# Kernel tuning notes

Hardware: AMD Instinct MI355X
Metric: run time of the kernel (lower is better)

Reference implementation:

```python
import jax, jax.numpy as jnp
import numpy as np

B, C, K, H, W = 8, 256, 19, 256, 256  # batch, input_nc, num_classes, spatial
NEG_SLOPE = 0.2


def setup_inputs() -> dict:
    key = jax.random.key(0)
    ks = jax.random.split(key, 12)
    x = jax.random.normal(ks[0], (B, C, H, W), jnp.float32)
    cam = jax.random.uniform(ks[1], (B, K, H, W), jnp.float32)
    gt = jax.random.randint(ks[2], (B, K), 0, 3, jnp.int32)
    gt_src = jax.random.uniform(ks[3], (B, K, K), jnp.float32)
    gt_tgt = jax.random.uniform(ks[4], (B, K, K), jnp.float32)
    weights = jax.random.uniform(ks[5], (B, K), jnp.float32)
    W1 = jax.random.normal(ks[6], (C, 2048), jnp.float32) * 0.02
    b1 = jnp.zeros((2048,), jnp.float32)
    W2 = jax.random.normal(ks[7], (2048, 512), jnp.float32) * 0.02
    b2 = jnp.zeros((512,), jnp.float32)
    Wc = jax.random.normal(ks[8], (512, 2 * K), jnp.float32) * 0.02
    bc = jnp.zeros((2 * K,), jnp.float32)
    return {"x": x, "cam": cam, "gt": gt, "gt_src": gt_src, "gt_tgt": gt_tgt,
            "weights": weights, "W1": W1, "b1": b1, "W2": W2, "b2": b2,
            "Wc": Wc, "bc": bc}


def reference(x, cam, gt, gt_src, gt_tgt, weights, W1, b1, W2, b2, Wc, bc):
    hw = x.shape[-1] * x.shape[-2]
    # cams_feature: mean over HW of cam[:,:,None]*x[:,None] -> [B, K, C]
    feat = jnp.einsum('bkhw,bchw->bkc', cam, x) / hw
    # Small MLP (self.D) + cls head, batched over all B*K rows; masking
    # replaces the per-sample ragged gather (extra rows are masked out below).
    h = jax.nn.leaky_relu(feat @ W1 + b1, NEG_SLOPE)
    h = jax.nn.leaky_relu(h @ W2 + b2, NEG_SLOPE)
    logits = h @ Wc + bc                      # [B, K, 2K]
    mask = (gt > 0).astype(logits.dtype)      # [B, K] selected rows
    lbl = jnp.concatenate([gt_src, gt_tgt], axis=-1)  # [B, K, 2K]
    logp = jax.nn.log_softmax(logits, axis=-1)
    ce = -(lbl * logp).sum(-1)                # [B, K]
    n = mask.sum(-1)                          # rows per sample
    sample_loss = (mask * weights * ce).sum(-1) / jnp.maximum(n, 1.0)
    lbl_sum = (mask[..., None] * lbl).sum((-2, -1))   # per-sample label mass
    valid = lbl_sum > 0                       # skip samples with lbl.sum()==0
    batch_size = x.shape[0]
    loss_img = jnp.where(valid, sample_loss, 0.0).sum() / batch_size
    match = (jnp.argmax(logits, -1) == jnp.argmax(lbl, -1)).astype(logits.dtype) * mask
    acc = jnp.where(valid, match.sum(-1), 0.0).sum()
    cnt = jnp.where(valid, lbl_sum, 0.0).sum()
    acc_img = acc / cnt * 100.0
    return jnp.stack([loss_img, acc_img])
```

## Files before the change

### kernel.cpp

```cpp
#include <hip/hip_runtime.h>
#include <stdint.h>

#define BB 8
#define CC 256
#define KK 19
#define HWN 65536
#define H1 2048
#define H2 512
#define NC 38
#define NEG 0.2f
#define NSL 16
#define HWS (HWN / NSL)
#define HWT 256
#define NCH (HWS / HWT)
#define CAMF4 (KK * HWT / 4)
#define NROW (BB * KK)

typedef float nat4 __attribute__((ext_vector_type(4)));

__device__ __forceinline__ void gload_lds16(const float4* g, float4* l) {
    __builtin_amdgcn_global_load_lds(
        (const __attribute__((address_space(1))) void*)g,
        (__attribute__((address_space(3))) void*)l, 16, 0, 0);
}

__global__ __launch_bounds__(256) void k_feat(const float* __restrict__ x,
                                              const float* __restrict__ cam,
                                              const int* __restrict__ gt,
                                              float* __restrict__ partial) {
    __shared__ float cams[2][KK * HWT];
    const int b  = blockIdx.y;
    const int cg = blockIdx.x & 15;
    const int sl = blockIdx.x >> 4;
    const int t  = threadIdx.x;
    const int w  = t >> 6;
    const int l  = t & 63;
    const int c0 = cg * 16 + w * 4;

    unsigned gtm = 0;
#pragma unroll
    for (int k = 0; k < KK; ++k)
        gtm |= (gt[b * KK + k] > 0) ? (1u << k) : 0u;

    const nat4*  __restrict__ x4  = reinterpret_cast<const nat4*>(x);
    const float4* __restrict__ cb4 = reinterpret_cast<const float4*>(cam) + (size_t)b * KK * (HWN / 4);
    const int slbase = sl * (HWS / 4);

    float acc[KK][4];
#pragma unroll
    for (int k = 0; k < KK; ++k)
#pragma unroll
        for (int c = 0; c < 4; ++c) acc[k][c] = 0.f;

    auto stage = [&](int buf, int ch) {
        const int f0 = slbase + ch * (HWT / 4);
#pragma unroll
        for (int j = 0; j < 5; ++j) {
            const int idx = w * 64 + j * 256;
            const int row = idx >> 6;
            if (idx < CAMF4 && ((gtm >> row) & 1)) {
                gload_lds16(cb4 + (size_t)row * (HWN / 4) + f0 + l,
                            ((float4*)cams[buf]) + idx + l);
            }
        }
    };
    auto loadx = [&](nat4 (&xv)[4], int ch) {
        const int f0 = slbase + ch * (HWT / 4);
#pragma unroll
        for (int c = 0; c < 4; ++c)
            xv[c] = __builtin_nontemporal_load(
                x4 + (size_t)(b * CC + c0 + c) * (HWN / 4) + f0 + l);
    };
    auto consume = [&](int buf, const nat4 (&xv)[4]) {
        const float4* cs = (const float4*)cams[buf];
#pragma unroll
        for (int k = 0; k < KK; ++k) {
            if ((gtm >> k) & 1) {
                const float4 cv = cs[k * (HWT / 4) + l];
#pragma unroll
                for (int c = 0; c < 4; ++c)
                    acc[k][c] = fmaf(xv[c].w, cv.w, fmaf(xv[c].z, cv.z,
                                fmaf(xv[c].y, cv.y, fmaf(xv[c].x, cv.x, acc[k][c]))));
            }
        }
    };

    nat4 xa[4], xb[4];
    loadx(xa, 0);
    stage(0, 0);
    __syncthreads();

#pragma unroll 1
    for (int ch = 0; ch < NCH; ch += 2) {
        loadx(xb, ch + 1);
        stage(1, ch + 1);
        consume(0, xa);
        __syncthreads();
        if (ch + 2 < NCH) { loadx(xa, ch + 2); stage(0, ch + 2); }
        consume(1, xb);
        __syncthreads();
    }

#pragma unroll
    for (int k = 0; k < KK; ++k) {
#pragma unroll
        for (int c = 0; c < 4; ++c) {
            float v = acc[k][c];
#pragma unroll
            for (int off = 32; off; off >>= 1) v += __shfl_xor(v, off, 64);
            if (l == 0)
                __builtin_nontemporal_store(v,
                    partial + (size_t)sl * (NROW * CC) +
                    (size_t)(b * KK + k) * CC + c0 + c);
        }
    }
}

__global__ __launch_bounds__(256) void k_mlp1(const float* __restrict__ partial,
                                              const float* __restrict__ W1,
                                              const float* __restrict__ b1,
                                              float* __restrict__ h1,
                                              float* __restrict__ scal) {
    __shared__ float fr[2][CC];
    const int r0 = blockIdx.y * 2;
    const int t  = threadIdx.x;
    if (blockIdx.x == 0 && blockIdx.y == 0 && t < 16) scal[t] = 0.f;

    float s0 = 0.f, s1 = 0.f;
#pragma unroll
    for (int slc = 0; slc < NSL; ++slc) {
        s0 += partial[((size_t)slc * NROW + r0) * CC + t];
        s1 += partial[((size_t)slc * NROW + r0 + 1) * CC + t];
    }
    fr[0][t] = s0 * (1.0f / (float)HWN);
    fr[1][t] = s1 * (1.0f / (float)HWN);
    __syncthreads();

    const int j = blockIdx.x * 256 + t;
    const float4* f0 = (const float4*)fr[0];
    const float4* f1 = (const float4*)fr[1];
    const float bias = b1[j];
    float a0 = bias, a1 = bias;
#pragma unroll 8
    for (int c4 = 0; c4 < CC / 4; ++c4) {
        const float4 v0 = f0[c4], v1 = f1[c4];
        const size_t cb = (size_t)(c4 * 4) * H1 + j;
        const float w0 = W1[cb], w1 = W1[cb + H1], w2 = W1[cb + 2 * H1], w3 = W1[cb + 3 * H1];
        a0 = fmaf(v0.x, w0, a0); a0 = fmaf(v0.y, w1, a0); a0 = fmaf(v0.z, w2, a0); a0 = fmaf(v0.w, w3, a0);
        a1 = fmaf(v1.x, w0, a1); a1 = fmaf(v1.y, w1, a1); a1 = fmaf(v1.z, w2, a1); a1 = fmaf(v1.w, w3, a1);
    }
    h1[(size_t)r0 * H1 + j]       = a0 > 0.f ? a0 : NEG * a0;
    h1[(size_t)(r0 + 1) * H1 + j] = a1 > 0.f ? a1 : NEG * a1;
}

__global__ __launch_bounds__(128) void k_mlp2p(const float* __restrict__ h1,
                                               const float* __restrict__ W2,
                                               float* __restrict__ part) {
    const int j  = blockIdx.x * 128 + threadIdx.x;
    const int r0 = blockIdx.y * 2;
    const int cb = blockIdx.z * 512;
    const float4* __restrict__ f0 = reinterpret_cast<const float4*>(h1 + (size_t)r0 * H1 + cb);
    const float4* __restrict__ f1 = reinterpret_cast<const float4*>(h1 + (size_t)(r0 + 1) * H1 + cb);

    float a0 = 0.f, a1 = 0.f;
#pragma unroll 8
    for (int c4 = 0; c4 < 128; ++c4) {
        const float4 v0 = f0[c4], v1 = f1[c4];
        const size_t wb = (size_t)(cb + c4 * 4) * H2 + j;
        const float w0 = W2[wb], w1 = W2[wb + H2], w2 = W2[wb + 2 * H2], w3 = W2[wb + 3 * H2];
        a0 = fmaf(v0.x, w0, a0); a0 = fmaf(v0.y, w1, a0); a0 = fmaf(v0.z, w2, a0); a0 = fmaf(v0.w, w3, a0);
        a1 = fmaf(v1.x, w0, a1); a1 = fmaf(v1.y, w1, a1); a1 = fmaf(v1.z, w2, a1); a1 = fmaf(v1.w, w3, a1);
    }
    part[((size_t)blockIdx.z * NROW + r0) * H2 + j]     = a0;
    part[((size_t)blockIdx.z * NROW + r0 + 1) * H2 + j] = a1;
}

__global__ __launch_bounds__(768) void k_loss(const float* __restrict__ part,
                                              const float* __restrict__ b2,
                                              const float* __restrict__ Wc,
                                              const float* __restrict__ bc,
                                              const int* __restrict__ gt,
                                              const float* __restrict__ gt_src,
                                              const float* __restrict__ gt_tgt,
                                              const float* __restrict__ wts,
                                              float* __restrict__ scal) {
    __shared__ float h2s[KK][H2];
    __shared__ float lg[KK][NC];
    __shared__ float rloss[KK], rmask[KK], rlbl[KK], rmatch[KK];

    const int b = blockIdx.x;
    const int t = threadIdx.x;

    for (int i = t; i < KK * H2; i += 768) {
        const int row = b * KK + (i >> 9);
        const int jj  = i & 511;
        float s = b2[jj];
#pragma unroll
        for (int p = 0; p < 4; ++p)
            s += part[((size_t)p * NROW + row) * H2 + jj];
        ((float*)h2s)[i] = s > 0.f ? s : NEG * s;
    }
    __syncthreads();

    if (t < KK * NC) {
        const int k = t / NC, j = t % NC;
        float acc = bc[j];
        for (int c = 0; c < H2; ++c) acc = fmaf(h2s[k][c], Wc[(size_t)c * NC + j], acc);
        lg[k][j] = acc;
    }
    __syncthreads();

    if (t < KK) {
        const int k = t;
        float m = -1e30f; int am = 0;
        for (int j = 0; j < NC; ++j) {
            float v = lg[k][j];
            if (v > m) { m = v; am = j; }
        }
        float se = 0.f, celbl = 0.f, lsum = 0.f, lm = -1e30f; int al = 0;
        for (int j = 0; j < NC; ++j) {
            float v = lg[k][j];
            se += expf(v - m);
            float lb = (j < KK) ? gt_src[((size_t)b * KK + k) * KK + j]
                                : gt_tgt[((size_t)b * KK + k) * KK + (j - KK)];
            celbl = fmaf(lb, v, celbl);
            lsum += lb;
            if (lb > lm) { lm = lb; al = j; }
        }
        float lse = m + logf(se);
        float ce = lse * lsum - celbl;
        float mask = (gt[b * KK + k] > 0) ? 1.f : 0.f;
        rloss[k]  = mask * wts[b * KK + k] * ce;
        rmask[k]  = mask;
        rlbl[k]   = mask * lsum;
        rmatch[k] = mask * ((am == al) ? 1.f : 0.f);
    }
    __syncthreads();

    if (t == 0) {
        float n = 0.f, sl = 0.f, ls = 0.f, mt = 0.f;
        for (int k = 0; k < KK; ++k) { n += rmask[k]; sl += rloss[k]; ls += rlbl[k]; mt += rmatch[k]; }
        float sample_loss = sl / fmaxf(n, 1.f);
        bool valid = ls > 0.f;
        atomicAdd(&scal[0], valid ? sample_loss : 0.f);
        atomicAdd(&scal[1], valid ? mt : 0.f);
        atomicAdd(&scal[2], valid ? ls : 0.f);
    }
}

__global__ void k_final(const float* __restrict__ scal, float* __restrict__ out) {
    out[0] = scal[0] / (float)BB;
    out[1] = scal[1] / scal[2] * 100.f;
}

extern "C" void kernel_launch(void* const* d_in, const int* in_sizes, int n_in,
                              void* d_out, int out_size, void* d_ws, size_t ws_size,
                              hipStream_t stream) {
    const float* x      = (const float*)d_in[0];
    const float* cam    = (const float*)d_in[1];
    const int*   gt     = (const int*)d_in[2];
    const float* gt_src = (const float*)d_in[3];
    const float* gt_tgt = (const float*)d_in[4];
    const float* wts    = (const float*)d_in[5];
    const float* W1     = (const float*)d_in[6];
    const float* b1     = (const float*)d_in[7];
    const float* W2     = (const float*)d_in[8];
    const float* b2     = (const float*)d_in[9];
    const float* Wc     = (const float*)d_in[10];
    const float* bc     = (const float*)d_in[11];

    float* ws      = (float*)d_ws;
    float* scal    = ws;
    float* partial = ws + 16;
    float* h1      = partial + (size_t)NSL * NROW * CC;
    float* part2   = h1 + (size_t)NROW * H1;

    dim3 g1(16 * NSL, BB);
    k_feat<<<g1, 256, 0, stream>>>(x, cam, gt, partial);
    dim3 g2(H1 / 256, NROW / 2);
    k_mlp1<<<g2, 256, 0, stream>>>(partial, W1, b1, h1, scal);
    dim3 g3(4, NROW / 2, 4);
    k_mlp2p<<<g3, 128, 0, stream>>>(h1, W2, part2);
    k_loss<<<BB, 768, 0, stream>>>(part2, b2, Wc, bc, gt, gt_src, gt_tgt, wts, scal);
    k_final<<<1, 1, 0, stream>>>(scal, (float*)d_out);
}
```

Measured before the change: 233.9 us.

## Skip masked rows in MLP kernels and halve HW slice count

The two MLP kernels now launch one block per row and return early when gt for that row is not positive, so rows the loss later masks out no longer read weights or do FMAs. The HW split of the feature reduction drops from 16 to 8 slices, which halves the partial-sum traffic but gives the feature kernel fewer blocks and longer per-block loops. Masked rows leave uninitialised h1 and part2 entries, so this is only safe if the loss kernel ignores those rows. Handling one row per block instead of two also means each weight load is reused for only one row.

After: 244.8 us. +4.7%, slower.

```diff
diff --git a/kernel.cpp b/kernel.cpp
--- a/kernel.cpp
+++ b/kernel.cpp
@@ -9,7 +9,7 @@
 #define H2 512
 #define NC 38
 #define NEG 0.2f
-#define NSL 16
+#define NSL 8
 #define HWS (HWN / NSL)
 #define HWT 256
 #define NCH (HWS / HWT)
@@ -119,60 +119,58 @@
 __global__ __launch_bounds__(256) void k_mlp1(const float* __restrict__ partial,
                                               const float* __restrict__ W1,
                                               const float* __restrict__ b1,
+                                              const int* __restrict__ gt,
                                               float* __restrict__ h1,
                                               float* __restrict__ scal) {
-    __shared__ float fr[2][CC];
-    const int r0 = blockIdx.y * 2;
-    const int t  = threadIdx.x;
+    __shared__ float fr[CC];
+    const int r = blockIdx.y;
+    const int t = threadIdx.x;
     if (blockIdx.x == 0 && blockIdx.y == 0 && t < 16) scal[t] = 0.f;
-
-    float s0 = 0.f, s1 = 0.f;
-#pragma unroll
-    for (int slc = 0; slc < NSL; ++slc) {
-        s0 += partial[((size_t)slc * NROW + r0) * CC + t];
-        s1 += partial[((size_t)slc * NROW + r0 + 1) * CC + t];
-    }
-    fr[0][t] = s0 * (1.0f / (float)HWN);
-    fr[1][t] = s1 * (1.0f / (float)HWN);
+    if (gt[r] <= 0) return;
+
+    float s0 = 0.f;
+#pragma unroll
+    for (int slc = 0; slc < NSL; ++slc)
+        s0 += partial[((size_t)slc * NROW + r) * CC + t];
+    fr[t] = s0 * (1.0f / (float)HWN);
     __syncthreads();
 
     const int j = blockIdx.x * 256 + t;
-    const float4* f0 = (const float4*)fr[0];
-    const float4* f1 = (const float4*)fr[1];
-    const float bias = b1[j];
-    float a0 = bias, a1 = bias;
+    const float4* f0 = (const float4*)fr;
+    float a0 = b1[j];
 #pragma unroll 8
     for (int c4 = 0; c4 < CC / 4; ++c4) {
-        const float4 v0 = f0[c4], v1 = f1[c4];
+        const float4 v0 = f0[c4];
         const size_t cb = (size_t)(c4 * 4) * H1 + j;
-        const float w0 = W1[cb], w1 = W1[cb + H1], w2 = W1[cb + 2 * H1], w3 = W1[cb + 3 * H1];
-        a0 = fmaf(v0.x, w0, a0); a0 = fmaf(v0.y, w1, a0); a0 = fmaf(v0.z, w2, a0); a0 = fmaf(v0.w, w3, a0);
-        a1 = fmaf(v1.x, w0, a1); a1 = fmaf(v1.y, w1, a1); a1 = fmaf(v1.z, w2, a1); a1 = fmaf(v1.w, w3, a1);
-    }
-    h1[(size_t)r0 * H1 + j]       = a0 > 0.f ? a0 : NEG * a0;
-    h1[(size_t)(r0 + 1) * H1 + j] = a1 > 0.f ? a1 : NEG * a1;
+        a0 = fmaf(v0.x, W1[cb], a0);
+        a0 = fmaf(v0.y, W1[cb + H1], a0);
+        a0 = fmaf(v0.z, W1[cb + 2 * H1], a0);
+        a0 = fmaf(v0.w, W1[cb + 3 * H1], a0);
+    }
+    h1[(size_t)r * H1 + j] = a0 > 0.f ? a0 : NEG * a0;
 }
 
 __global__ __launch_bounds__(128) void k_mlp2p(const float* __restrict__ h1,
                                                const float* __restrict__ W2,
+                                               const int* __restrict__ gt,
                                                float* __restrict__ part) {
+    const int r = blockIdx.y;
+    if (gt[r] <= 0) return;
     const int j  = blockIdx.x * 128 + threadIdx.x;
-    const int r0 = blockIdx.y * 2;
     const int cb = blockIdx.z * 512;
-    const float4* __restrict__ f0 = reinterpret_cast<const float4*>(h1 + (size_t)r0 * H1 + cb);
-    const float4* __restrict__ f1 = reinterpret_cast<const float4*>(h1 + (size_t)(r0 + 1) * H1 + cb);
-
-    float a0 = 0.f, a1 = 0.f;
+    const float4* __restrict__ f0 = reinterpret_cast<const float4*>(h1 + (size_t)r * H1 + cb);
+
+    float a0 = 0.f;
 #pragma unroll 8
     for (int c4 = 0; c4 < 128; ++c4) {
-        const float4 v0 = f0[c4], v1 = f1[c4];
+        const float4 v0 = f0[c4];
         const size_t wb = (size_t)(cb + c4 * 4) * H2 + j;
-        const float w0 = W2[wb], w1 = W2[wb + H2], w2 = W2[wb + 2 * H2], w3 = W2[wb + 3 * H2];
-        a0 = fmaf(v0.x, w0, a0); a0 = fmaf(v0.y, w1, a0); a0 = fmaf(v0.z, w2, a0); a0 = fmaf(v0.w, w3, a0);
-        a1 = fmaf(v1.x, w0, a1); a1 = fmaf(v1.y, w1, a1); a1 = fmaf(v1.z, w2, a1); a1 = fmaf(v1.w, w3, a1);
-    }
-    part[((size_t)blockIdx.z * NROW + r0) * H2 + j]     = a0;
-    part[((size_t)blockIdx.z * NROW + r0 + 1) * H2 + j] = a1;
+        a0 = fmaf(v0.x, W2[wb], a0);
+        a0 = fmaf(v0.y, W2[wb + H2], a0);
+        a0 = fmaf(v0.z, W2[wb + 2 * H2], a0);
+        a0 = fmaf(v0.w, W2[wb + 3 * H2], a0);
+    }
+    part[((size_t)blockIdx.z * NROW + r) * H2 + j] = a0;
 }
 
 __global__ __launch_bounds__(768) void k_loss(const float* __restrict__ part,
@@ -277,10 +275,10 @@
 
     dim3 g1(16 * NSL, BB);
     k_feat<<<g1, 256, 0, stream>>>(x, cam, gt, partial);
-    dim3 g2(H1 / 256, NROW / 2);
-    k_mlp1<<<g2, 256, 0, stream>>>(partial, W1, b1, h1, scal);
-    dim3 g3(4, NROW / 2, 4);
-    k_mlp2p<<<g3, 128, 0, stream>>>(h1, W2, part2);
+    dim3 g2(H1 / 256, NROW);
+    k_mlp1<<<g2, 256, 0, stream>>>(partial, W1, b1, gt, h1, scal);
+    dim3 g3(4, NROW, 4);
+    k_mlp2p<<<g3, 128, 0, stream>>>(h1, W2, gt, part2);
     k_loss<<<BB, 768, 0, stream>>>(part2, b2, Wc, bc, gt, gt_src, gt_tgt, wts, scal);
     k_final<<<1, 1, 0, stream>>>(scal, (float*)d_out);
 }
```
